# Kernel tuning notes

Hardware: AMD Instinct MI355X
Metric: run time of the kernel (lower is better)

The kernel has to match this reference:

```python
import jax, jax.numpy as jnp
import numpy as np

NUM_EMBEDDINGS = 8192
EMBEDDING_DIM = 64
N_VOXELS = 32768


def setup_inputs() -> dict:
    key = jax.random.key(0)
    k1, k2 = jax.random.split(key)
    z = jax.random.normal(k1, (N_VOXELS, EMBEDDING_DIM), dtype=jnp.float32)
    codebook = jax.random.normal(k2, (NUM_EMBEDDINGS, EMBEDDING_DIM), dtype=jnp.float32)
    return {"z": z, "codebook": codebook}


def reference(z, codebook):
    # Squared euclidean distances [N, K]; argmin is identical to argmin of cdist.
    # d2 = ||z||^2 - 2 z E^T + ||E||^2
    z_sq = jnp.sum(z * z, axis=1, keepdims=True)            # [N, 1]
    e_sq = jnp.sum(codebook * codebook, axis=1)              # [K]
    d2 = z_sq - 2.0 * (z @ codebook.T) + e_sq[None, :]       # [N, K]
    encoding_indices = jnp.argmin(d2, axis=1)                # [N] int

    quantized_feats = codebook[encoding_indices]             # [N, D] gather

    sg = jax.lax.stop_gradient
    commitment_loss = jnp.mean((z - sg(quantized_feats)) ** 2)
    vq_loss = jnp.mean((quantized_feats - sg(z)) ** 2)

    # Straight-through estimator
    quantized = z + sg(quantized_feats - z)                  # [N, D]

    return quantized, vq_loss, commitment_loss, encoding_indices
```

## Files before the change

kernel.cpp:

```cpp
#include <hip/hip_runtime.h>
#include <math.h>

#define N_VOX 32768
#define N_EMB 8192
#define DIM 64
#define NCHUNK 8
#define CODES_PER_CHUNK (N_EMB / NCHUNK)
#define TILES_PER_CHUNK (CODES_PER_CHUNK / 32)
#define NTILES (N_EMB / 32)
#define TILE_BYTES 8192
#define CHUNK_BYTES (TILES_PER_CHUNK * TILE_BYTES)

typedef _Float16 half8 __attribute__((ext_vector_type(8)));
typedef float floatx16 __attribute__((ext_vector_type(16)));

#define FP16_MIN_NORMAL 6.1035156e-5f
#define LO_SCALE 2048.0f

__global__ __launch_bounds__(256) void cbprep_kernel(const float* __restrict__ cb,
                                                     char* __restrict__ stream,
                                                     float* __restrict__ esq,
                                                     float* __restrict__ c0arr) {
    int t    = blockIdx.x * 256 + threadIdx.x;
    int l    = t & 63;
    int m    = l & 31;
    int kg   = l >> 5;
    int tile = t >> 6;
    char* tbase = stream + (size_t)tile * TILE_BYTES;
    int code = tile * 32 + m;

    float ss = 0.f;
    #pragma unroll
    for (int o = 0; o < 4; ++o) {
        const float* p = cb + (size_t)code * DIM + o * 16 + kg * 8;
        half8 h, lo;
        #pragma unroll
        for (int j = 0; j < 8; ++j) {
            float x = p[j];
            ss = fmaf(x, x, ss);
            _Float16 hi = (_Float16)x;
            float hf = (float)hi;
            if (fabsf(hf) < FP16_MIN_NORMAL) { hi = (_Float16)0.f; hf = 0.f; }
            h[j]  = hi;
            lo[j] = (_Float16)((x - hf) * LO_SCALE);
        }
        *(half8*)(tbase +        o * 1024 + l * 16) = h;
        *(half8*)(tbase + 4096 + o * 1024 + l * 16) = lo;
    }
    ss += __shfl_xor(ss, 32, 64);
    if (kg == 0) {
        esq[code]   = ss;
        c0arr[code] = -1024.0f * ss;
    }
}

__global__ __launch_bounds__(256, 3) void scan_kernel(const float* __restrict__ z,
                                                      const char* __restrict__ stream,
                                                      const float* __restrict__ c0arr,
                                                      int* __restrict__ cand_idx) {
    __shared__ __align__(16) char lds[2 * TILE_BYTES];
    int tid   = threadIdx.x;
    int l     = tid & 63;
    int w     = tid >> 6;
    int chunk = blockIdx.x & (NCHUNK - 1);
    int rg    = blockIdx.x >> 3;
    int m     = l & 31;
    int kg    = l >> 5;
    int rowBase = rg * 128 + w * 32;

    half8 zh[4], zl[4], zhs[4];
    const float* zrow = z + (size_t)(rowBase + m) * DIM + kg * 8;
    #pragma unroll
    for (int o = 0; o < 4; ++o) {
        const float* p = zrow + o * 16;
        #pragma unroll
        for (int j = 0; j < 8; ++j) {
            float x = p[j];
            _Float16 hi = (_Float16)x;
            float hf = (float)hi;
            if (fabsf(hf) < FP16_MIN_NORMAL) { hi = (_Float16)0.f; hf = 0.f; }
            zh[o][j] = hi;
            zl[o][j] = (_Float16)((x - hf) * LO_SCALE);
        }
        zhs[o] = zh[o] * (_Float16)2048.0f;
    }

    const char*  sbase = stream + (size_t)chunk * CHUNK_BYTES;
    const float* c0p   = c0arr + chunk * CODES_PER_CHUNK;

    float best[16];
    int   bt[16];
    #pragma unroll
    for (int i = 0; i < 16; ++i) { best[i] = -3.4e38f; bt[i] = 0; }

#define STAGE(gt, lb)                                                              \
    do {                                                                           \
        _Pragma("unroll")                                                          \
        for (int _s = w; _s < 8; _s += 4) {                                        \
            const char* _g = (gt) + _s * 1024 + l * 16;                            \
            char*       _d = (lb) + _s * 1024 + l * 16;                            \
            __builtin_amdgcn_global_load_lds(                                      \
                (const __attribute__((address_space(1))) void*)_g,                 \
                (__attribute__((address_space(3))) void*)_d, 16, 0, 0);            \
        }                                                                          \
    } while (0)

    STAGE(sbase, lds);
    float c0 = c0p[m];
    __syncthreads();

    for (int t = 0; t < TILES_PER_CHUNK; ++t) {
        if (t + 1 < TILES_PER_CHUNK)
            STAGE(sbase + (size_t)(t + 1) * TILE_BYTES, lds + ((t + 1) & 1) * TILE_BYTES);
        float c0n = (t + 1 < TILES_PER_CHUNK) ? c0p[(t + 1) * 32 + m] : 0.f;

        const char* lb = lds + (t & 1) * TILE_BYTES;
        half8 bh[4], bl[4];
        #pragma unroll
        for (int o = 0; o < 4; ++o) {
            bh[o] = *(const half8*)(lb +        o * 1024 + l * 16);
            bl[o] = *(const half8*)(lb + 4096 + o * 1024 + l * 16);
        }

        floatx16 acc;
        #pragma unroll
        for (int i = 0; i < 16; ++i) acc[i] = c0;
        #pragma unroll
        for (int o = 0; o < 4; ++o) {
            acc = __builtin_amdgcn_mfma_f32_32x32x16_f16(zhs[o], bh[o], acc, 0, 0, 0);
            acc = __builtin_amdgcn_mfma_f32_32x32x16_f16(zl[o],  bh[o], acc, 0, 0, 0);
            acc = __builtin_amdgcn_mfma_f32_32x32x16_f16(zh[o],  bl[o], acc, 0, 0, 0);
        }
        #pragma unroll
        for (int i = 0; i < 16; ++i)
            if (acc[i] > best[i]) { best[i] = acc[i]; bt[i] = t; }

        c0 = c0n;
        __syncthreads();
    }
#undef STAGE

    #pragma unroll
    for (int i = 0; i < 16; ++i) {
        float v  = best[i];
        int   id = bt[i] * 32 + m;
        #pragma unroll
        for (int off = 1; off < 32; off <<= 1) {
            float ov = __shfl_xor(v, off, 64);
            int   oi = __shfl_xor(id, off, 64);
            if (ov > v || (ov == v && oi < id)) { v = ov; id = oi; }
        }
        if (m == 0) {
            int row = rowBase + (i & 3) + 8 * (i >> 2) + 4 * kg;
            cand_idx[chunk * N_VOX + row] = chunk * CODES_PER_CHUNK + id;
        }
    }
}

__global__ __launch_bounds__(256) void finalize_kernel(const float* __restrict__ z,
                                                       const float* __restrict__ cb,
                                                       const float* __restrict__ esq,
                                                       const int* __restrict__ cand_idx,
                                                       float* __restrict__ out,
                                                       float* __restrict__ partials) {
    int tid  = threadIdx.x;
    int l    = tid & 63;
    int w    = tid >> 6;
    int row  = blockIdx.x * 4 + w;
    int c    = l >> 3;
    int s    = l & 7;

    int id = cand_idx[c * N_VOX + row];

    const float4* zp = (const float4*)(z  + (size_t)row * DIM + s * 8);
    const float4* ep = (const float4*)(cb + (size_t)id  * DIM + s * 8);
    float4 z0 = zp[0], z1 = zp[1], e0 = ep[0], e1 = ep[1];
    float p = z0.x*e0.x + z0.y*e0.y + z0.z*e0.z + z0.w*e0.w
            + z1.x*e1.x + z1.y*e1.y + z1.z*e1.z + z1.w*e1.w;
    #pragma unroll
    for (int off = 1; off < 8; off <<= 1)
        p += __shfl_xor(p, off, 8);

    float score = esq[id] - 2.0f * p;
    #pragma unroll
    for (int off = 8; off < 64; off <<= 1) {
        float ov = __shfl_xor(score, off, 64);
        int   oi = __shfl_xor(id, off, 64);
        if (ov < score || (ov == score && oi < id)) { score = ov; id = oi; }
    }

    if (l == 0)
        out[(size_t)N_VOX * DIM + 2 + row] = (float)id;

    float zv = z[(size_t)row * DIM + l];
    float qv = cb[(size_t)id * DIM + l];
    float d  = qv - zv;
    out[(size_t)row * DIM + l] = zv + d;
    float ss = d * d;
    #pragma unroll
    for (int off = 1; off < 64; off <<= 1)
        ss += __shfl_xor(ss, off, 64);

    __shared__ float red[4];
    if (l == 0) red[w] = ss;
    __syncthreads();
    if (tid == 0)
        partials[blockIdx.x] = (red[0] + red[1]) + (red[2] + red[3]);
}

__global__ __launch_bounds__(256) void loss_kernel(const float* __restrict__ partials,
                                                   float* __restrict__ out) {
    float s = 0.f;
    #pragma unroll
    for (int i = 0; i < 32; ++i)
        s += partials[threadIdx.x + i * 256];
    __shared__ float red[256];
    red[threadIdx.x] = s;
    __syncthreads();
    #pragma unroll
    for (int st = 128; st > 0; st >>= 1) {
        if (threadIdx.x < st) red[threadIdx.x] += red[threadIdx.x + st];
        __syncthreads();
    }
    if (threadIdx.x == 0) {
        float mean = red[0] / (float)((size_t)N_VOX * DIM);
        out[(size_t)N_VOX * DIM + 0] = mean;
        out[(size_t)N_VOX * DIM + 1] = mean;
    }
}

extern "C" void kernel_launch(void* const* d_in, const int* in_sizes, int n_in,
                              void* d_out, int out_size, void* d_ws, size_t ws_size,
                              hipStream_t stream) {
    const float* z  = (const float*)d_in[0];
    const float* cb = (const float*)d_in[1];
    float* out = (float*)d_out;

    char*  bstream  = (char*)d_ws;
    float* esq      = (float*)(bstream + (size_t)NTILES * TILE_BYTES);
    float* c0arr    = esq + N_EMB;
    int*   cand_idx = (int*)(c0arr + N_EMB);
    float* partials = (float*)(cand_idx + (size_t)NCHUNK * N_VOX);

    cbprep_kernel  <<<dim3(NTILES * 64 / 256), dim3(256), 0, stream>>>(cb, bstream, esq, c0arr);
    scan_kernel    <<<dim3((N_VOX / 128) * NCHUNK), dim3(256), 0, stream>>>(z, bstream, c0arr, cand_idx);
    finalize_kernel<<<dim3(N_VOX / 4), dim3(256), 0, stream>>>(z, cb, esq, cand_idx, out, partials);
    loss_kernel    <<<1, 256, 0, stream>>>(partials, out);
}
```

Before: 191.0 us.

## Stage two codebook tiles per sync round and fuse loss reduction via atomics

```diff
diff --git a/kernel.cpp b/kernel.cpp
--- a/kernel.cpp
+++ b/kernel.cpp
@@ -7,8 +7,10 @@
 #define NCHUNK 8
 #define CODES_PER_CHUNK (N_EMB / NCHUNK)
 #define TILES_PER_CHUNK (CODES_PER_CHUNK / 32)
+#define NROUND (TILES_PER_CHUNK / 2)
 #define NTILES (N_EMB / 32)
 #define TILE_BYTES 8192
+#define ROUND_BYTES (2 * TILE_BYTES)
 #define CHUNK_BYTES (TILES_PER_CHUNK * TILE_BYTES)
 
 typedef _Float16 half8 __attribute__((ext_vector_type(8)));
@@ -17,15 +19,14 @@
 #define FP16_MIN_NORMAL 6.1035156e-5f
 #define LO_SCALE 2048.0f
 
-__global__ __launch_bounds__(256) void cbprep_kernel(const float* __restrict__ cb,
-                                                     char* __restrict__ stream,
-                                                     float* __restrict__ esq,
-                                                     float* __restrict__ c0arr) {
-    int t    = blockIdx.x * 256 + threadIdx.x;
-    int l    = t & 63;
+__global__ __launch_bounds__(64) void cbprep_kernel(const float* __restrict__ cb,
+                                                    char* __restrict__ stream,
+                                                    float* __restrict__ esq,
+                                                    float* __restrict__ c0arr) {
+    int l    = threadIdx.x;
     int m    = l & 31;
     int kg   = l >> 5;
-    int tile = t >> 6;
+    int tile = blockIdx.x;
     char* tbase = stream + (size_t)tile * TILE_BYTES;
     int code = tile * 32 + m;
 
@@ -58,7 +59,7 @@
                                                       const char* __restrict__ stream,
                                                       const float* __restrict__ c0arr,
                                                       int* __restrict__ cand_idx) {
-    __shared__ __align__(16) char lds[2 * TILE_BYTES];
+    __shared__ __align__(16) char lds[2 * ROUND_BYTES];
     int tid   = threadIdx.x;
     int l     = tid & 63;
     int w     = tid >> 6;
@@ -93,11 +94,11 @@
     #pragma unroll
     for (int i = 0; i < 16; ++i) { best[i] = -3.4e38f; bt[i] = 0; }
 
-#define STAGE(gt, lb)                                                              \
+#define STAGE(gr, lb)                                                              \
     do {                                                                           \
         _Pragma("unroll")                                                          \
-        for (int _s = w; _s < 8; _s += 4) {                                        \
-            const char* _g = (gt) + _s * 1024 + l * 16;                            \
+        for (int _s = w; _s < 16; _s += 4) {                                       \
+            const char* _g = (gr) + _s * 1024 + l * 16;                            \
             char*       _d = (lb) + _s * 1024 + l * 16;                            \
             __builtin_amdgcn_global_load_lds(                                      \
                 (const __attribute__((address_space(1))) void*)_g,                 \
@@ -105,40 +106,48 @@
         }                                                                          \
     } while (0)
 
+#define PROC(lb, C0, tt)                                                           \
+    do {                                                                           \
+        half8 _bh[4], _bl[4];                                                      \
+        _Pragma("unroll")                                                          \
+        for (int _o = 0; _o < 4; ++_o) {                                           \
+            _bh[_o] = *(const half8*)((lb) +        _o * 1024 + l * 16);           \
+            _bl[_o] = *(const half8*)((lb) + 4096 + _o * 1024 + l * 16);           \
+        }                                                                          \
+        floatx16 _acc;                                                             \
+        _Pragma("unroll")                                                          \
+        for (int _i = 0; _i < 16; ++_i) _acc[_i] = (C0);                           \
+        _Pragma("unroll")                                                          \
+        for (int _o = 0; _o < 4; ++_o) {                                           \
+            _acc = __builtin_amdgcn_mfma_f32_32x32x16_f16(zhs[_o], _bh[_o], _acc, 0, 0, 0); \
+            _acc = __builtin_amdgcn_mfma_f32_32x32x16_f16(zl[_o],  _bh[_o], _acc, 0, 0, 0); \
+            _acc = __builtin_amdgcn_mfma_f32_32x32x16_f16(zh[_o],  _bl[_o], _acc, 0, 0, 0); \
+        }                                                                          \
+        _Pragma("unroll")                                                          \
+        for (int _i = 0; _i < 16; ++_i)                                            \
+            if (_acc[_i] > best[_i]) { best[_i] = _acc[_i]; bt[_i] = (tt); }       \
+    } while (0)
+
     STAGE(sbase, lds);
-    float c0 = c0p[m];
+    float c0a = c0p[m];
+    float c0b = c0p[32 + m];
     __syncthreads();
 
-    for (int t = 0; t < TILES_PER_CHUNK; ++t) {
-        if (t + 1 < TILES_PER_CHUNK)
-            STAGE(sbase + (size_t)(t + 1) * TILE_BYTES, lds + ((t + 1) & 1) * TILE_BYTES);
-        float c0n = (t + 1 < TILES_PER_CHUNK) ? c0p[(t + 1) * 32 + m] : 0.f;
-
-        const char* lb = lds + (t & 1) * TILE_BYTES;
-        half8 bh[4], bl[4];
-        #pragma unroll
-        for (int o = 0; o < 4; ++o) {
-            bh[o] = *(const half8*)(lb +        o * 1024 + l * 16);
-            bl[o] = *(const half8*)(lb + 4096 + o * 1024 + l * 16);
-        }
-
-        floatx16 acc;
-        #pragma unroll
-        for (int i = 0; i < 16; ++i) acc[i] = c0;
-        #pragma unroll
-        for (int o = 0; o < 4; ++o) {
-            acc = __builtin_amdgcn_mfma_f32_32x32x16_f16(zhs[o], bh[o], acc, 0, 0, 0);
-            acc = __builtin_amdgcn_mfma_f32_32x32x16_f16(zl[o],  bh[o], acc, 0, 0, 0);
-            acc = __builtin_amdgcn_mfma_f32_32x32x16_f16(zh[o],  bl[o], acc, 0, 0, 0);
-        }
-        #pragma unroll
-        for (int i = 0; i < 16; ++i)
-            if (acc[i] > best[i]) { best[i] = acc[i]; bt[i] = t; }
-
-        c0 = c0n;
+    for (int r = 0; r < NROUND; ++r) {
+        if (r + 1 < NROUND)
+            STAGE(sbase + (size_t)(r + 1) * ROUND_BYTES, lds + ((r + 1) & 1) * ROUND_BYTES);
+        float c0an = (r + 1 < NROUND) ? c0p[(2 * r + 2) * 32 + m] : 0.f;
+        float c0bn = (r + 1 < NROUND) ? c0p[(2 * r + 3) * 32 + m] : 0.f;
+
+        const char* lb = lds + (r & 1) * ROUND_BYTES;
+        PROC(lb,              c0a, 2 * r);
+        PROC(lb + TILE_BYTES, c0b, 2 * r + 1);
+
+        c0a = c0an; c0b = c0bn;
         __syncthreads();
     }
 #undef STAGE
+#undef PROC
 
     #pragma unroll
     for (int i = 0; i < 16; ++i) {
@@ -162,7 +171,8 @@
                                                        const float* __restrict__ esq,
                                                        const int* __restrict__ cand_idx,
                                                        float* __restrict__ out,
-                                                       float* __restrict__ partials) {
+                                                       float* __restrict__ acc_sum,
+                                                       unsigned int* __restrict__ acc_cnt) {
     int tid  = threadIdx.x;
     int l    = tid & 63;
     int w    = tid >> 6;
@@ -204,28 +214,17 @@
     __shared__ float red[4];
     if (l == 0) red[w] = ss;
     __syncthreads();
-    if (tid == 0)
-        partials[blockIdx.x] = (red[0] + red[1]) + (red[2] + red[3]);
-}
-
-__global__ __launch_bounds__(256) void loss_kernel(const float* __restrict__ partials,
-                                                   float* __restrict__ out) {
-    float s = 0.f;
-    #pragma unroll
-    for (int i = 0; i < 32; ++i)
-        s += partials[threadIdx.x + i * 256];
-    __shared__ float red[256];
-    red[threadIdx.x] = s;
-    __syncthreads();
-    #pragma unroll
-    for (int st = 128; st > 0; st >>= 1) {
-        if (threadIdx.x < st) red[threadIdx.x] += red[threadIdx.x + st];
-        __syncthreads();
-    }
-    if (threadIdx.x == 0) {
-        float mean = red[0] / (float)((size_t)N_VOX * DIM);
-        out[(size_t)N_VOX * DIM + 0] = mean;
-        out[(size_t)N_VOX * DIM + 1] = mean;
+    if (tid == 0) {
+        float part = (red[0] + red[1]) + (red[2] + red[3]);
+        atomicAdd(acc_sum, part);
+        __threadfence();
+        unsigned int old = atomicAdd(acc_cnt, 1u);
+        if (old == gridDim.x - 1) {
+            float total = atomicAdd(acc_sum, 0.0f);
+            float mean  = total / (float)((size_t)N_VOX * DIM);
+            out[(size_t)N_VOX * DIM + 0] = mean;
+            out[(size_t)N_VOX * DIM + 1] = mean;
+        }
     }
 }
 
@@ -240,10 +239,12 @@
     float* esq      = (float*)(bstream + (size_t)NTILES * TILE_BYTES);
     float* c0arr    = esq + N_EMB;
     int*   cand_idx = (int*)(c0arr + N_EMB);
-    float* partials = (float*)(cand_idx + (size_t)NCHUNK * N_VOX);
-
-    cbprep_kernel  <<<dim3(NTILES * 64 / 256), dim3(256), 0, stream>>>(cb, bstream, esq, c0arr);
+    float* acc_sum  = (float*)(cand_idx + (size_t)NCHUNK * N_VOX);
+    unsigned int* acc_cnt = (unsigned int*)(acc_sum + 1);
+
+    hipMemsetAsync(acc_sum, 0, 8, stream);
+    cbprep_kernel  <<<dim3(NTILES), dim3(64), 0, stream>>>(cb, bstream, esq, c0arr);
     scan_kernel    <<<dim3((N_VOX / 128) * NCHUNK), dim3(256), 0, stream>>>(z, bstream, c0arr, cand_idx);
-    finalize_kernel<<<dim3(N_VOX / 4), dim3(256), 0, stream>>>(z, cb, esq, cand_idx, out, partials);
-    loss_kernel    <<<1, 256, 0, stream>>>(partials, out);
-}
+    finalize_kernel<<<dim3(N_VOX / 4), dim3(256), 0, stream>>>(z, cb, esq, cand_idx, out, acc_sum,
+                                                               (unsigned int*)acc_cnt);
+}
```

New measurement: 394.7 us. 107% more time.
